# Optimization experiments

Measured on AMD Instinct MI355X. Metric: run time of the kernel, lower is better.

## Reference

```python
import jax, jax.numpy as jnp
import numpy as np

N_HEAD, D_MODEL, D_HEAD = 16, 1024, 64
BSZ, SEQLEN = 2, 2048
ROPE_BASE = 10000.0


def _rope_tables(seqlen, d_head, base=ROPE_BASE):
    # freqs_cis = exp(i * t * theta_j), theta_j = base^(-2j/d_head)
    inv_freq = 1.0 / (base ** (np.arange(0, d_head, 2, dtype=np.float32) / d_head))
    t = np.arange(seqlen, dtype=np.float32)
    ang = np.outer(t, inv_freq)  # [S, d_head//2]
    return jnp.asarray(np.cos(ang)), jnp.asarray(np.sin(ang))


def setup_inputs() -> dict:
    key = jax.random.key(0)
    ks = jax.random.split(key, 5)
    x = jax.random.normal(ks[0], (BSZ, SEQLEN, D_MODEL), dtype=jnp.float32)
    freqs_cos, freqs_sin = _rope_tables(SEQLEN, D_HEAD)
    scale = 0.02
    # weights stored as (in, out) so projection is x @ w
    wq = jax.random.normal(ks[1], (D_MODEL, N_HEAD * D_HEAD), dtype=jnp.float32) * scale
    wk = jax.random.normal(ks[2], (D_MODEL, N_HEAD * D_HEAD), dtype=jnp.float32) * scale
    wv = jax.random.normal(ks[3], (D_MODEL, N_HEAD * D_HEAD), dtype=jnp.float32) * scale
    wo = jax.random.normal(ks[4], (N_HEAD * D_HEAD, D_MODEL), dtype=jnp.float32) * scale
    return {"x": x, "freqs_cos": freqs_cos, "freqs_sin": freqs_sin,
            "wq": wq, "wk": wk, "wv": wv, "wo": wo}


def _apply_rope(t, cos, sin):
    # t: [B, S, H, Dh]; complex pairs are consecutive elements (x0 + i*x1)
    B, S, H, Dh = t.shape
    tf = t.astype(jnp.float32).reshape(B, S, H, Dh // 2, 2)
    t0, t1 = tf[..., 0], tf[..., 1]
    c = cos[None, :, None, :]  # [1, S, 1, Dh//2]
    s = sin[None, :, None, :]
    o0 = t0 * c - t1 * s
    o1 = t0 * s + t1 * c
    return jnp.stack([o0, o1], axis=-1).reshape(B, S, H, Dh).astype(t.dtype)


def reference(x, freqs_cos, freqs_sin, wq, wk, wv, wo):
    B, S, _ = x.shape
    H, Dh = N_HEAD, D_HEAD
    q = jnp.einsum('bsd,de->bse', x, wq).reshape(B, S, H, Dh)
    k = jnp.einsum('bsd,de->bse', x, wk).reshape(B, S, H, Dh)
    v = jnp.einsum('bsd,de->bse', x, wv).reshape(B, S, H, Dh)
    q = _apply_rope(q, freqs_cos, freqs_sin)
    k = _apply_rope(k, freqs_cos, freqs_sin)
    # [B, H, S, Dh]
    q = q.transpose(0, 2, 1, 3)
    k = k.transpose(0, 2, 1, 3)
    v = v.transpose(0, 2, 1, 3)
    scores = jnp.einsum('bhqd,bhkd->bhqk', q, k) / jnp.sqrt(jnp.float32(Dh))
    probs = jax.nn.softmax(scores.astype(jnp.float32), axis=-1).astype(q.dtype)
    out = jnp.einsum('bhqk,bhkd->bhqd', probs, v)  # [B, H, S, Dh]
    out = out.transpose(0, 2, 1, 3).reshape(B, S, H * Dh)
    return jnp.einsum('bse,ed->bsd', out, wo)
```

## Files before the change

kernel.cpp:

```cpp
#include <hip/hip_runtime.h>
#include <math.h>

#define BSZ 2
#define SEQ 2048
#define NH 16
#define DH 64
#define DM 1024
#define HD 1024

typedef _Float16 h16;
typedef _Float16 half8 __attribute__((ext_vector_type(8)));
typedef _Float16 half4 __attribute__((ext_vector_type(4)));
typedef float f32x4 __attribute__((ext_vector_type(4)));
typedef unsigned int u32;
typedef unsigned int u32x2v __attribute__((ext_vector_type(2)));
typedef unsigned int u32x4v __attribute__((ext_vector_type(4)));

__device__ __forceinline__ f32x4 mfma16(half8 a, half8 b, f32x4 c) {
    return __builtin_amdgcn_mfma_f32_16x16x32_f16(a, b, c, 0, 0, 0);
}

__device__ __forceinline__ void async_copy16(h16* lds, const h16* g) {
    __builtin_amdgcn_global_load_lds(
        (const __attribute__((address_space(1))) unsigned int*)g,
        (__attribute__((address_space(3))) unsigned int*)lds, 16, 0, 0);
}

#define SWZ(cb, r) ((((cb) ^ ((r) & 7)) * 8))

#define OBA(r, c) ((r) * 64 + ((((c) >> 2) ^ ((r) & 15)) << 2))

#define EXP2(x) __builtin_amdgcn_exp2f(x)

__device__ __forceinline__ u32 pack2(float a, float b) {
    h16 lo = (h16)a, hi = (h16)b;
    return (u32)__builtin_bit_cast(unsigned short, lo) |
           ((u32)__builtin_bit_cast(unsigned short, hi) << 16);
}

__device__ __forceinline__ void pl32swap(u32& a, u32& b) {
#if __has_builtin(__builtin_amdgcn_permlane32_swap)
    u32x2v r = __builtin_amdgcn_permlane32_swap(a, b, false, false);
    a = r.x; b = r.y;
#else
    u32 sa = __builtin_amdgcn_ds_swizzle(a, 0x801F);
    u32 sb = __builtin_amdgcn_ds_swizzle(b, 0x801F);
    bool hi = (threadIdx.x & 32) != 0;
    u32 na = hi ? sb : a;
    u32 nb = hi ? b : sa;
    a = na; b = nb;
#endif
}

__device__ __forceinline__ void pl16swap(u32& a, u32& b) {
#if __has_builtin(__builtin_amdgcn_permlane16_swap)
    u32x2v r = __builtin_amdgcn_permlane16_swap(a, b, false, false);
    a = r.x; b = r.y;
#else
    u32 sa = __builtin_amdgcn_ds_swizzle(a, 0x401F);
    u32 sb = __builtin_amdgcn_ds_swizzle(b, 0x401F);
    bool hi = (threadIdx.x & 16) != 0;
    u32 na = hi ? sb : a;
    u32 nb = hi ? b : sa;
    a = na; b = nb;
#endif
}

__global__ __launch_bounds__(256) void prep_kernel(
    const float* __restrict__ x, const float* __restrict__ wq,
    const float* __restrict__ wk, const float* __restrict__ wv,
    const float* __restrict__ wo,
    h16* __restrict__ x16, h16* __restrict__ wt)
{
    const int z = blockIdx.z;
    const int t = threadIdx.x;
    if (z == 4) {
        int flat = blockIdx.y * 16 + blockIdx.x;
#pragma unroll
        for (int i = 0; i < 8; ++i) {
            int idx = flat * 16384 + i * 2048 + t * 8;
            float4 a = *(const float4*)&x[idx];
            float4 b = *(const float4*)&x[idx + 4];
            half8 o;
            o[0] = (h16)a.x; o[1] = (h16)a.y; o[2] = (h16)a.z; o[3] = (h16)a.w;
            o[4] = (h16)b.x; o[5] = (h16)b.y; o[6] = (h16)b.z; o[7] = (h16)b.w;
            *(half8*)&x16[idx] = o;
        }
        return;
    }
    const float* w = (z == 0) ? wq : (z == 1) ? wk : (z == 2) ? wv : wo;
    h16* ot = wt + (size_t)z * DM * DM;
    __shared__ float tile[64][68];
    const int k0 = blockIdx.y * 64, n0 = blockIdx.x * 64;
    const int r = t >> 2, c4 = (t & 3) * 16;
#pragma unroll
    for (int i = 0; i < 16; i += 4) {
        float4 v = *(const float4*)&w[(size_t)(k0 + r) * DM + n0 + c4 + i];
        tile[r][c4 + i + 0] = v.x; tile[r][c4 + i + 1] = v.y;
        tile[r][c4 + i + 2] = v.z; tile[r][c4 + i + 3] = v.w;
    }
    __syncthreads();
#pragma unroll
    for (int g = 0; g < 2; ++g) {
        half8 hh;
#pragma unroll
        for (int j = 0; j < 8; ++j)
            hh[j] = (h16)tile[c4 + g * 8 + j][r];
        *(half8*)&ot[(size_t)(n0 + r) * DM + k0 + c4 + g * 8] = hh;
    }
}

__global__ __launch_bounds__(512, 4) void qkv_kernel(
    const h16* __restrict__ x16, const h16* __restrict__ wt,
    const float* __restrict__ fcos, const float* __restrict__ fsin,
    h16* __restrict__ Q16, h16* __restrict__ K16, h16* __restrict__ VT16)
{
    const int id  = (blockIdx.z * 32 + blockIdx.y) * 8 + blockIdx.x;
    const int swz = (id & 7) * 96 + (id >> 3);
    const int z   = swz >> 8;
    const int m0  = ((swz >> 3) & 31) * 128;
    const int n0  = (swz & 7) * 128;

    const h16* __restrict__ bw = wt + (size_t)z * DM * DM;

    __shared__ h16 smem[32768];
    h16* Vt = smem;

    const int t  = threadIdx.x;
    const int w  = t >> 6, ln = t & 63;
    const int L  = ln & 15, U = ln >> 4;
    const int wm = (w & 3) * 32;
    const int wn = (w >> 2) * 64;

    const int sr  = ln >> 3;
    const int scb = (ln & 7) ^ sr;

    f32x4 acc[2][4];
#pragma unroll
    for (int i = 0; i < 2; ++i)
#pragma unroll
        for (int j = 0; j < 4; ++j) acc[i][j] = (f32x4)0.0f;

#pragma unroll
    for (int c = 0; c < 2; ++c) {
        int rb = w * 16 + c * 8;
        async_copy16(&smem[rb * 64],        &x16[(size_t)(m0 + rb + sr) * DM + scb * 8]);
        async_copy16(&smem[8192 + rb * 64], &bw [(size_t)(n0 + rb + sr) * DM + scb * 8]);
    }

    for (int k0 = 0; k0 < DM; k0 += 64) {
        const int buf = (k0 >> 6) & 1;
        h16* As = smem + buf * 16384;
        h16* Bs = As + 8192;

        asm volatile("s_waitcnt vmcnt(0)" ::: "memory");
        __builtin_amdgcn_s_barrier();
        __builtin_amdgcn_sched_barrier(0);

        if (k0 + 64 < DM) {
            h16* An = smem + (buf ^ 1) * 16384;
#pragma unroll
            for (int c = 0; c < 2; ++c) {
                int rb = w * 16 + c * 8;
                async_copy16(&An[rb * 64],
                             &x16[(size_t)(m0 + rb + sr) * DM + k0 + 64 + scb * 8]);
                async_copy16(&An[8192 + rb * 64],
                             &bw [(size_t)(n0 + rb + sr) * DM + k0 + 64 + scb * 8]);
            }
        }

        __builtin_amdgcn_s_setprio(1);
#pragma unroll
        for (int ks = 0; ks < 2; ++ks) {
            half8 af[2], bf[4];
#pragma unroll
            for (int mt = 0; mt < 2; ++mt)
                af[mt] = *(const half8*)&As[(wm + mt * 16 + L) * 64 + SWZ(ks * 4 + U, L)];
#pragma unroll
            for (int nt = 0; nt < 4; ++nt)
                bf[nt] = *(const half8*)&Bs[(wn + nt * 16 + L) * 64 + SWZ(ks * 4 + U, L)];
#pragma unroll
            for (int mt = 0; mt < 2; ++mt)
#pragma unroll
                for (int nt = 0; nt < 4; ++nt)
                    acc[mt][nt] = mfma16(bf[nt], af[mt], acc[mt][nt]);
        }
        __builtin_amdgcn_s_setprio(0);
    }

    const int b = m0 >> 11;
    const int sbase = m0 & 2047;

    if (z < 2) {
        const float sc = (z == 0) ? 0.125f * 1.44269504088896f : 1.0f;
#pragma unroll
        for (int mt = 0; mt < 2; ++mt) {
            int s = sbase + wm + mt * 16 + L;
            const float* ct = &fcos[s * 32];
            const float* st = &fsin[s * 32];
#pragma unroll
            for (int nt = 0; nt < 4; ++nt) {
                int nl = n0 + wn + nt * 16 + U * 4;
                int d = nl & 63, h = nl >> 6;
                int pd = d >> 1;
                float cv0 = ct[pd], sv0 = st[pd];
                float cv1 = ct[pd + 1], sv1 = st[pd + 1];
                float v0 = acc[mt][nt][0], v1 = acc[mt][nt][1];
                float v2 = acc[mt][nt][2], v3 = acc[mt][nt][3];
                float o0 = (v0 * cv0 - v1 * sv0) * sc;
                float o1 = (v0 * sv0 + v1 * cv0) * sc;
                float o2 = (v2 * cv1 - v3 * sv1) * sc;
                float o3 = (v2 * sv1 + v3 * cv1) * sc;
                size_t addr = ((size_t)(b * NH + h) * SEQ + s) * DH + d;
                half4 kk;
                kk[0] = (h16)o0; kk[1] = (h16)o1; kk[2] = (h16)o2; kk[3] = (h16)o3;
                if (z == 0) *(half4*)&Q16[addr] = kk;
                else        *(half4*)&K16[addr] = kk;
            }
        }
    } else {
        __syncthreads();
#pragma unroll
        for (int mt = 0; mt < 2; ++mt)
#pragma unroll
            for (int nt = 0; nt < 4; ++nt)
#pragma unroll
                for (int r = 0; r < 4; ++r) {
                    int nloc = wn + nt * 16 + U * 4 + r;
                    int sloc = wm + mt * 16 + L;
                    Vt[nloc * 136 + sloc] = (h16)acc[mt][nt][r];
                }
        __syncthreads();
#pragma unroll
        for (int i = 0; i < 4; ++i) {
            int c = i * 512 + t;
            int dl = c >> 4;
            int s8 = (c & 15) * 8;
            half8 vv = *(const half8*)&Vt[dl * 136 + s8];
            int n = n0 + dl;
            int d = n & 63, h = n >> 6;
            *(half8*)&VT16[((size_t)(b * NH + h) * DH + d) * SEQ + sbase + s8] = vv;
        }
    }
}

__global__ __launch_bounds__(512, 4) void attn_kernel(
    const h16* __restrict__ Q16, const h16* __restrict__ K16,
    const h16* __restrict__ VT16, h16* __restrict__ A16)
{
    __shared__ h16 smem[32768];
    float* lbuf = (float*)(smem + 16384);
    float* Obuf = (float*)smem;

    const int t = threadIdx.x, w = t >> 6, ln = t & 63;
    const int L = ln & 15, U = ln >> 4;
    const int pair = w >> 1, half = w & 1;
    const int qw = pair * 32, kh = half * 64;

    const int id  = blockIdx.y * 16 + blockIdx.x;
    const int swz = (id & 7) * 64 + (id >> 3);
    const int q0  = (swz & 15) * 128;
    const int bh  = swz >> 4;
    const size_t base = (size_t)bh * SEQ * DH;

    half8 qf[2][2];
#pragma unroll
    for (int qb = 0; qb < 2; ++qb)
#pragma unroll
        for (int ks = 0; ks < 2; ++ks)
            qf[qb][ks] = *(const half8*)&Q16[base + (size_t)(q0 + qw + qb * 16 + L) * DH + ks * 32 + U * 8];

    half8 one8;
#pragma unroll
    for (int i = 0; i < 8; ++i) one8[i] = (h16)1.0f;

    f32x4 O[4][2];
    f32x4 lsum[2];
#pragma unroll
    for (int dt = 0; dt < 4; ++dt)
#pragma unroll
        for (int qb = 0; qb < 2; ++qb) O[dt][qb] = (f32x4)0.0f;
    lsum[0] = (f32x4)0.0f;
    lsum[1] = (f32x4)0.0f;

    const int sr  = ln >> 3;
    const int scb = (ln & 7) ^ sr;

#pragma unroll
    for (int c = 0; c < 2; ++c) {
        int rbk = c * 64 + w * 8;
        async_copy16(&smem[rbk * 64], &K16[base + (size_t)(rbk + sr) * DH + scb * 8]);
    }
#pragma unroll
    for (int c = 0; c < 2; ++c) {
        int rv = (w * 2 + c) * 4;
        int c16 = (ln & 15) ^ ((rv + U) & 15);
        async_copy16(&smem[16384 + rv * 128], &VT16[base + (size_t)(rv + U) * SEQ + c16 * 8]);
    }

    for (int j0 = 0; j0 < SEQ; j0 += 128) {
        const int buf = (j0 >> 7) & 1;
        h16* Kcur  = smem + buf * 8192;
        h16* VTcur = smem + 16384 + buf * 8192;

        __builtin_amdgcn_sched_barrier(0);
        asm volatile("s_waitcnt vmcnt(0)" ::: "memory");
        __builtin_amdgcn_s_barrier();
        __builtin_amdgcn_sched_barrier(0);

        if (j0 + 128 < SEQ) {
            h16* Knxt  = smem + (buf ^ 1) * 8192;
            h16* Vnxt  = smem + 16384 + (buf ^ 1) * 8192;
#pragma unroll
            for (int c = 0; c < 2; ++c) {
                int rbk = c * 64 + w * 8;
                async_copy16(&Knxt[rbk * 64],
                             &K16[base + (size_t)(j0 + 128 + rbk + sr) * DH + scb * 8]);
            }
#pragma unroll
            for (int c = 0; c < 2; ++c) {
                int rv = (w * 2 + c) * 4;
                int c16 = (ln & 15) ^ ((rv + U) & 15);
                async_copy16(&Vnxt[rv * 128],
                             &VT16[base + (size_t)(rv + U) * SEQ + (j0 + 128) + c16 * 8]);
            }
        }

        f32x4 S[4][2];
        __builtin_amdgcn_s_setprio(1);
#pragma unroll
        for (int nt = 0; nt < 4; ++nt) {
            S[nt][0] = (f32x4)0.0f;
            S[nt][1] = (f32x4)0.0f;
#pragma unroll
            for (int ks = 0; ks < 2; ++ks) {
                half8 kf = *(const half8*)&Kcur[(kh + nt * 16 + L) * 64 + SWZ(ks * 4 + U, L)];
                S[nt][0] = mfma16(kf, qf[0][ks], S[nt][0]);
                S[nt][1] = mfma16(kf, qf[1][ks], S[nt][1]);
            }
        }
        __builtin_amdgcn_s_setprio(0);

        half8 pf[2][2];
#pragma unroll
        for (int qb = 0; qb < 2; ++qb) {
            u32 X[2][2][2];
#pragma unroll
            for (int k5 = 0; k5 < 2; ++k5)
#pragma unroll
                for (int p = 0; p < 2; ++p) {
                    u32 a = pack2(EXP2(S[k5 * 2 + 0][qb][2 * p]),
                                  EXP2(S[k5 * 2 + 0][qb][2 * p + 1]));
                    u32 b = pack2(EXP2(S[k5 * 2 + 1][qb][2 * p]),
                                  EXP2(S[k5 * 2 + 1][qb][2 * p + 1]));
                    pl32swap(a, b);
                    X[k5][0][p] = a; X[k5][1][p] = b;
                }
#pragma unroll
            for (int k5 = 0; k5 < 2; ++k5) {
                u32x4v uv;
#pragma unroll
                for (int p = 0; p < 2; ++p) {
                    u32 a = X[k5][0][p], b = X[k5][1][p];
                    pl16swap(a, b);
                    uv[p]     = a;
                    uv[2 + p] = b;
                }
                pf[qb][k5] = __builtin_bit_cast(half8, uv);
            }
        }

        __builtin_amdgcn_s_setprio(1);
#pragma unroll
        for (int dt = 0; dt < 4; ++dt)
#pragma unroll
            for (int ks2 = 0; ks2 < 2; ++ks2) {
                half8 vf = *(const half8*)&VTcur[(dt * 16 + L) * 128 + ((half * 8 + ks2 * 4 + U) ^ L) * 8];
                O[dt][0] = mfma16(vf, pf[0][ks2], O[dt][0]);
                O[dt][1] = mfma16(vf, pf[1][ks2], O[dt][1]);
            }
#pragma unroll
        for (int ks2 = 0; ks2 < 2; ++ks2) {
            lsum[0] = mfma16(one8, pf[0][ks2], lsum[0]);
            lsum[1] = mfma16(one8, pf[1][ks2], lsum[1]);
        }
        __builtin_amdgcn_s_setprio(0);
    }

    if (U == 0) {
        lbuf[w * 32 + L]      = lsum[0][0];
        lbuf[w * 32 + 16 + L] = lsum[1][0];
    }
    __syncthreads();
    const int pw = w ^ 1;
    float l_tot[2];
    l_tot[0] = lsum[0][0] + lbuf[pw * 32 + L];
    l_tot[1] = lsum[1][0] + lbuf[pw * 32 + 16 + L];

    if (half) {
#pragma unroll
        for (int qb = 0; qb < 2; ++qb)
#pragma unroll
            for (int dt = 0; dt < 4; ++dt)
                *(f32x4*)&Obuf[OBA(qw + qb * 16 + L, dt * 16 + U * 4)] = O[dt][qb];
    }
    __syncthreads();
    if (!half) {
        const int b = bh >> 4, hh = bh & 15;
#pragma unroll
        for (int qb = 0; qb < 2; ++qb) {
            float inv = 1.0f / l_tot[qb];
            int s = q0 + qw + qb * 16 + L;
#pragma unroll
            for (int dt = 0; dt < 4; ++dt) {
                f32x4 op = *(const f32x4*)&Obuf[OBA(qw + qb * 16 + L, dt * 16 + U * 4)];
                half4 o4;
#pragma unroll
                for (int r = 0; r < 4; ++r)
                    o4[r] = (h16)((O[dt][qb][r] + op[r]) * inv);
                *(half4*)&A16[(size_t)(b * SEQ + s) * HD + hh * DH + dt * 16 + U * 4] = o4;
            }
        }
    }
}

__global__ __launch_bounds__(512, 4) void oproj_kernel(
    const h16* __restrict__ A16, const h16* __restrict__ bw,
    float* __restrict__ out)
{
    __shared__ h16 smem[24576];

    const int id  = blockIdx.y * 16 + blockIdx.x;
    const int swz = (id & 7) * 64 + (id >> 3);
    const int n0  = (swz & 15) * 64;
    const int m0  = (swz >> 4) * 128;

    const int t  = threadIdx.x;
    const int w  = t >> 6, ln = t & 63;
    const int L  = ln & 15, U = ln >> 4;

    const int sr  = ln >> 3;
    const int scb = (ln & 7) ^ sr;

    f32x4 acc[4];
#pragma unroll
    for (int j = 0; j < 4; ++j) acc[j] = (f32x4)0.0f;

#pragma unroll
    for (int c = 0; c < 2; ++c) {
        int rb = w * 16 + c * 8;
        async_copy16(&smem[rb * 64], &A16[(size_t)(m0 + rb + sr) * DM + scb * 8]);
    }
    async_copy16(&smem[8192 + (w * 8) * 64], &bw[(size_t)(n0 + w * 8 + sr) * DM + scb * 8]);

    for (int k0 = 0; k0 < DM; k0 += 64) {
        const int buf = (k0 >> 6) & 1;
        h16* As = smem + buf * 12288;
        h16* Bs = As + 8192;

        asm volatile("s_waitcnt vmcnt(0)" ::: "memory");
        __builtin_amdgcn_s_barrier();
        __builtin_amdgcn_sched_barrier(0);

        if (k0 + 64 < DM) {
            h16* An = smem + (buf ^ 1) * 12288;
#pragma unroll
            for (int c = 0; c < 2; ++c) {
                int rb = w * 16 + c * 8;
                async_copy16(&An[rb * 64],
                             &A16[(size_t)(m0 + rb + sr) * DM + k0 + 64 + scb * 8]);
            }
            async_copy16(&An[8192 + (w * 8) * 64],
                         &bw[(size_t)(n0 + w * 8 + sr) * DM + k0 + 64 + scb * 8]);
        }

        __builtin_amdgcn_s_setprio(1);
#pragma unroll
        for (int ks = 0; ks < 2; ++ks) {
            half8 af, bf[4];
            af = *(const half8*)&As[(w * 16 + L) * 64 + SWZ(ks * 4 + U, L)];
#pragma unroll
            for (int nt = 0; nt < 4; ++nt)
                bf[nt] = *(const half8*)&Bs[(nt * 16 + L) * 64 + SWZ(ks * 4 + U, L)];
#pragma unroll
            for (int nt = 0; nt < 4; ++nt)
                acc[nt] = mfma16(af, bf[nt], acc[nt]);
        }
        __builtin_amdgcn_s_setprio(0);
    }

#pragma unroll
    for (int nt = 0; nt < 4; ++nt)
#pragma unroll
        for (int r = 0; r < 4; ++r) {
            int row = m0 + w * 16 + U * 4 + r;
            int col = n0 + nt * 16 + L;
            out[(size_t)row * DM + col] = acc[nt][r];
        }
}

extern "C" void kernel_launch(void* const* d_in, const int* in_sizes, int n_in,
                              void* d_out, int out_size, void* d_ws, size_t ws_size,
                              hipStream_t stream)
{
    const float* x    = (const float*)d_in[0];
    const float* fcos = (const float*)d_in[1];
    const float* fsin = (const float*)d_in[2];
    const float* wq   = (const float*)d_in[3];
    const float* wk   = (const float*)d_in[4];
    const float* wv   = (const float*)d_in[5];
    const float* wo   = (const float*)d_in[6];
    float* out = (float*)d_out;

    const size_t M4 = (size_t)4 * 1024 * 1024;
    h16* x16  = (h16*)d_ws;
    h16* wt   = x16 + M4;
    h16* Q16  = wt + M4;
    h16* K16  = Q16 + M4;
    h16* VT16 = K16 + M4;
    h16* A16  = VT16 + M4;

    prep_kernel<<<dim3(16, 16, 5), 256, 0, stream>>>(x, wq, wk, wv, wo, x16, wt);
    qkv_kernel<<<dim3(8, 32, 3), 512, 0, stream>>>(x16, wt, fcos, fsin,
                                                   Q16, K16, VT16);
    attn_kernel<<<dim3(16, 32), 512, 0, stream>>>(Q16, K16, VT16, A16);
    oproj_kernel<<<dim3(16, 32), 512, 0, stream>>>(A16, wt + 3 * (size_t)DM * DM, out);
}
```

Baseline: 183.2 us.

## Single-buffer K in attention for occupancy; triple-buffer oproj loads

The attention kernel now holds K in a single LDS buffer. The next K tile is prefetched after the QK^T MMAs finish reading it, behind an extra barrier, which shrinks LDS so launch bounds can rise to 6 blocks per CU. The output-projection kernel moves from double to triple buffering with a two-tile-ahead prefetch and a partial vmcnt wait. The FP16 packing now uses the packed round-toward-zero convert. The costs are an extra barrier per attention iteration, less latency hiding for K loads, more LDS in oproj, and slightly different rounding in P.

```diff
diff --git a/kernel.cpp b/kernel.cpp
--- a/kernel.cpp
+++ b/kernel.cpp
@@ -33,9 +33,8 @@
 #define EXP2(x) __builtin_amdgcn_exp2f(x)
 
 __device__ __forceinline__ u32 pack2(float a, float b) {
-    h16 lo = (h16)a, hi = (h16)b;
-    return (u32)__builtin_bit_cast(unsigned short, lo) |
-           ((u32)__builtin_bit_cast(unsigned short, hi) << 16);
+    auto p = __builtin_amdgcn_cvt_pkrtz(a, b);
+    return __builtin_bit_cast(u32, p);
 }
 
 __device__ __forceinline__ void pl32swap(u32& a, u32& b) {
@@ -153,6 +152,7 @@
         h16* As = smem + buf * 16384;
         h16* Bs = As + 8192;
 
+        __builtin_amdgcn_sched_barrier(0);
         asm volatile("s_waitcnt vmcnt(0)" ::: "memory");
         __builtin_amdgcn_s_barrier();
         __builtin_amdgcn_sched_barrier(0);
@@ -244,13 +244,13 @@
     }
 }
 
-__global__ __launch_bounds__(512, 4) void attn_kernel(
+__global__ __launch_bounds__(512, 6) void attn_kernel(
     const h16* __restrict__ Q16, const h16* __restrict__ K16,
     const h16* __restrict__ VT16, h16* __restrict__ A16)
 {
-    __shared__ h16 smem[32768];
-    float* lbuf = (float*)(smem + 16384);
-    float* Obuf = (float*)smem;
+    __shared__ h16 smem[24576];
+    float* lbuf = (float*)smem;
+    float* Obuf = (float*)(smem + 8192);
 
     const int t = threadIdx.x, w = t >> 6, ln = t & 63;
     const int L = ln & 15, U = ln >> 4;
@@ -295,13 +295,12 @@
     for (int c = 0; c < 2; ++c) {
         int rv = (w * 2 + c) * 4;
         int c16 = (ln & 15) ^ ((rv + U) & 15);
-        async_copy16(&smem[16384 + rv * 128], &VT16[base + (size_t)(rv + U) * SEQ + c16 * 8]);
+        async_copy16(&smem[8192 + rv * 128], &VT16[base + (size_t)(rv + U) * SEQ + c16 * 8]);
     }
 
     for (int j0 = 0; j0 < SEQ; j0 += 128) {
         const int buf = (j0 >> 7) & 1;
-        h16* Kcur  = smem + buf * 8192;
-        h16* VTcur = smem + 16384 + buf * 8192;
+        h16* VTcur = smem + 8192 + buf * 8192;
 
         __builtin_amdgcn_sched_barrier(0);
         asm volatile("s_waitcnt vmcnt(0)" ::: "memory");
@@ -309,14 +308,7 @@
         __builtin_amdgcn_sched_barrier(0);
 
         if (j0 + 128 < SEQ) {
-            h16* Knxt  = smem + (buf ^ 1) * 8192;
-            h16* Vnxt  = smem + 16384 + (buf ^ 1) * 8192;
-#pragma unroll
-            for (int c = 0; c < 2; ++c) {
-                int rbk = c * 64 + w * 8;
-                async_copy16(&Knxt[rbk * 64],
-                             &K16[base + (size_t)(j0 + 128 + rbk + sr) * DH + scb * 8]);
-            }
+            h16* Vnxt = smem + 8192 + (buf ^ 1) * 8192;
 #pragma unroll
             for (int c = 0; c < 2; ++c) {
                 int rv = (w * 2 + c) * 4;
@@ -334,12 +326,26 @@
             S[nt][1] = (f32x4)0.0f;
 #pragma unroll
             for (int ks = 0; ks < 2; ++ks) {
-                half8 kf = *(const half8*)&Kcur[(kh + nt * 16 + L) * 64 + SWZ(ks * 4 + U, L)];
+                half8 kf = *(const half8*)&smem[(kh + nt * 16 + L) * 64 + SWZ(ks * 4 + U, L)];
                 S[nt][0] = mfma16(kf, qf[0][ks], S[nt][0]);
                 S[nt][1] = mfma16(kf, qf[1][ks], S[nt][1]);
             }
         }
         __builtin_amdgcn_s_setprio(0);
+
+        __builtin_amdgcn_sched_barrier(0);
+        asm volatile("s_waitcnt lgkmcnt(0)" ::: "memory");
+        __builtin_amdgcn_sched_barrier(0);
+        __builtin_amdgcn_s_barrier();
+
+        if (j0 + 128 < SEQ) {
+#pragma unroll
+            for (int c = 0; c < 2; ++c) {
+                int rbk = c * 64 + w * 8;
+                async_copy16(&smem[rbk * 64],
+                             &K16[base + (size_t)(j0 + 128 + rbk + sr) * DH + scb * 8]);
+            }
+        }
 
         half8 pf[2][2];
 #pragma unroll
@@ -428,7 +434,7 @@
     const h16* __restrict__ A16, const h16* __restrict__ bw,
     float* __restrict__ out)
 {
-    __shared__ h16 smem[24576];
+    __shared__ h16 smem[36864];
 
     const int id  = blockIdx.y * 16 + blockIdx.x;
     const int swz = (id & 7) * 64 + (id >> 3);
@@ -446,32 +452,34 @@
 #pragma unroll
     for (int j = 0; j < 4; ++j) acc[j] = (f32x4)0.0f;
 
-#pragma unroll
-    for (int c = 0; c < 2; ++c) {
-        int rb = w * 16 + c * 8;
-        async_copy16(&smem[rb * 64], &A16[(size_t)(m0 + rb + sr) * DM + scb * 8]);
-    }
-    async_copy16(&smem[8192 + (w * 8) * 64], &bw[(size_t)(n0 + w * 8 + sr) * DM + scb * 8]);
-
-    for (int k0 = 0; k0 < DM; k0 += 64) {
-        const int buf = (k0 >> 6) & 1;
+    auto stage = [&](int buf, int kk) {
+        h16* dst = smem + buf * 12288;
+#pragma unroll
+        for (int c = 0; c < 2; ++c) {
+            int rb = w * 16 + c * 8;
+            async_copy16(&dst[rb * 64], &A16[(size_t)(m0 + rb + sr) * DM + kk + scb * 8]);
+        }
+        async_copy16(&dst[8192 + (w * 8) * 64], &bw[(size_t)(n0 + w * 8 + sr) * DM + kk + scb * 8]);
+    };
+
+    stage(0, 0);
+    stage(1, 64);
+
+    int step = 0;
+    for (int k0 = 0; k0 < DM; k0 += 64, ++step) {
+        const int buf = step - (step / 3) * 3;
         h16* As = smem + buf * 12288;
         h16* Bs = As + 8192;
 
-        asm volatile("s_waitcnt vmcnt(0)" ::: "memory");
+        __builtin_amdgcn_sched_barrier(0);
+        if (k0 + 64 < DM) asm volatile("s_waitcnt vmcnt(3)" ::: "memory");
+        else              asm volatile("s_waitcnt vmcnt(0)" ::: "memory");
         __builtin_amdgcn_s_barrier();
         __builtin_amdgcn_sched_barrier(0);
 
-        if (k0 + 64 < DM) {
-            h16* An = smem + (buf ^ 1) * 12288;
-#pragma unroll
-            for (int c = 0; c < 2; ++c) {
-                int rb = w * 16 + c * 8;
-                async_copy16(&An[rb * 64],
-                             &A16[(size_t)(m0 + rb + sr) * DM + k0 + 64 + scb * 8]);
-            }
-            async_copy16(&An[8192 + (w * 8) * 64],
-                         &bw[(size_t)(n0 + w * 8 + sr) * DM + k0 + 64 + scb * 8]);
+        if (k0 + 128 < DM) {
+            int nb = step + 2;
+            stage(nb - (nb / 3) * 3, k0 + 128);
         }
 
         __builtin_amdgcn_s_setprio(1);
```

New measurement: 297.0 us. +62.1%, slower.
